# Optimization experiments

Measured on AMD Instinct MI355X. Metric: run time of the kernel, lower is better.

The kernel has to match this reference:

```python
import jax, jax.numpy as jnp
import numpy as np


def _mlp(x, W1, b1, W2, b2):
    # x: (B, M, T); torch MLPLayer: transpose(1,2) -> Linear -> Linear -> LeakyReLU -> transpose back
    h = jnp.einsum('bmt,hm->bht', x, W1) + b1[None, :, None]   # (B, H, T)
    y = jnp.einsum('bht,oh->bot', h, W2) + b2[None, :, None]   # (B, M, T)
    return jax.nn.leaky_relu(y, negative_slope=0.01)


def _calc_attn(q, k, v):
    # q: (B, M, Tq), k: (B, M, Tk), v: (B, M, Tk)
    Tq = q.shape[-1]
    qk = jnp.einsum('bmq,bmk->bqk', q, k)                       # (B, Tq, Tk)
    eye = jnp.eye(Tq, dtype=qk.dtype)                           # broadcasts: (Tq,Tq) or (1,1)
    logits = jnp.exp(qk - qk * eye / jnp.sqrt(jnp.asarray(Tq, qk.dtype)))
    scores = jax.nn.softmax(logits, axis=-1)
    return jnp.einsum('bqk,bmk->bmq', scores, v)                # (B, M, Tq)


def setup_inputs() -> dict:
    key = jax.random.key(0)
    B, M, T, H = 16, 128, 2048, 512
    ks = jax.random.split(key, 14)
    s = 0.02
    inp = {
        'pattern': jax.random.normal(ks[0], (B, M, T), jnp.float32),
        'value': jax.random.normal(ks[1], (B, M, T), jnp.float32),
        'kernel_size': 33,
    }
    names = ['q', 'k', 'o']
    for i, n in enumerate(names):
        inp['W%s1' % n] = jax.random.normal(ks[2 + 4 * i], (H, M), jnp.float32) * s
        inp['b%s1' % n] = jax.random.normal(ks[3 + 4 * i], (H,), jnp.float32) * s
        inp['W%s2' % n] = jax.random.normal(ks[4 + 4 * i], (M, H), jnp.float32) * s
        inp['b%s2' % n] = jax.random.normal(ks[5 + 4 * i], (M,), jnp.float32) * s
    return inp


def reference(pattern, value, kernel_size, Wq1, bq1, Wq2, bq2, Wk1, bk1, Wk2, bk2, Wo1, bo1, Wo2, bo2):
    query = _mlp(pattern, Wq1, bq1, Wq2, bq2)
    key = _mlp(pattern, Wk1, bk1, Wk2, bk2)
    # full (internal) attention
    attn_in = _calc_attn(query, key, value)                     # (B, M, T)
    rep_in = _mlp(attn_in, Wo1, bo1, Wo2, bo2)
    # windowed (external) attention
    T = query.shape[-1]
    cu = (kernel_size - 1) // 2
    q_w = query[..., T - 1 - cu : T - cu]                       # (B, M, 1)
    k_w = key[..., kernel_size - cu - 1 : T - cu - 2]           # (B, M, T-k-1)
    v_w = value[..., kernel_size : T - 1]                       # (B, M, T-k-1)
    attn_ex = _calc_attn(q_w, k_w, v_w)                         # (B, M, 1)
    rep_ex = _mlp(attn_ex, Wo1, bo1, Wo2, bo2)
    return jnp.concatenate([rep_in, rep_ex], axis=-1)           # (B, M, T+1)
```

## Files before the change

### kernel.cpp

```cpp
#include <hip/hip_runtime.h>
#include <math.h>

#define B_    16
#define M_    128
#define T_    2048
#define H_    512
#define TOUT_ 2049

typedef unsigned short u16;
typedef unsigned int   u32;
typedef __bf16 bf16x8 __attribute__((ext_vector_type(8)));
typedef float  f32x16 __attribute__((ext_vector_type(16)));
typedef u32    u32x4  __attribute__((ext_vector_type(4)));
typedef u32    u32x2  __attribute__((ext_vector_type(2)));

#define A_OFF     0
#define C_OFF     16384
#define MEAN_OFF  16896
#define AQKBF_OFF 19200
#define AOBF_OFF  35584
#define QT_OFF    43776
#define KT_OFF    (43776 + 2097152)
#define VB_OFF    (43776 + 2 * 2097152)

static __device__ __forceinline__ u16 f2bf(float f) {
  u32 u = __float_as_uint(f);
  u = (u + 0x7FFFu + ((u >> 16) & 1u)) >> 16;
  return (u16)u;
}
static __device__ __forceinline__ u32 pk2(float lo, float hi) {
  return (u32)f2bf(lo) | ((u32)f2bf(hi) << 16);
}
static __device__ __forceinline__ bf16x8 ldfrag(const u16* p) {
  return __builtin_bit_cast(bf16x8, *(const u32x4*)p);
}

__global__ __launch_bounds__(128) void fuse_weights_all(
    const float* __restrict__ W1q, const float* __restrict__ b1q,
    const float* __restrict__ W2q, const float* __restrict__ b2q,
    const float* __restrict__ W1k, const float* __restrict__ b1k,
    const float* __restrict__ W2k, const float* __restrict__ b2k,
    const float* __restrict__ W1o, const float* __restrict__ b1o,
    const float* __restrict__ W2o, const float* __restrict__ b2o,
    float* __restrict__ A, float* __restrict__ c,
    u16* __restrict__ Aqk_bf, u16* __restrict__ Ao_bf) {
  __shared__ float w2row[H_];
  int which = blockIdx.x >> 7;
  int o = blockIdx.x & 127;
  const float* W1 = which == 0 ? W1q : which == 1 ? W1k : W1o;
  const float* b1 = which == 0 ? b1q : which == 1 ? b1k : b1o;
  const float* W2 = which == 0 ? W2q : which == 1 ? W2k : W2o;
  const float* b2 = which == 0 ? b2q : which == 1 ? b2k : b2o;
  int m = threadIdx.x;
  for (int h = m; h < H_; h += 128) w2row[h] = W2[o * H_ + h];
  __syncthreads();
  float acc = 0.f;
#pragma unroll 8
  for (int h = 0; h < H_; ++h) acc = fmaf(w2row[h], W1[h * M_ + m], acc);
  u16 ab = f2bf(acc);
  if (which == 0)      Aqk_bf[o * 128 + m] = ab;
  else if (which == 1) Aqk_bf[(128 + o) * 128 + m] = ab;
  else               { Ao_bf[o * 128 + m] = ab; A[o * M_ + m] = acc; }
  if (m < 64) {
    float cc = 0.f;
    for (int h = m; h < H_; h += 64) cc = fmaf(w2row[h], b1[h], cc);
#pragma unroll
    for (int off = 32; off > 0; off >>= 1) cc += __shfl_down(cc, off, 64);
    if (m == 0) c[which * 128 + o] = cc + b2[o];
  }
}

#define XS 68

__global__ __launch_bounds__(256) void prep_kernel(
    const float* __restrict__ pattern, const u16* __restrict__ Aqk_bf,
    const float* __restrict__ cqk, u16* __restrict__ qT, u16* __restrict__ kT,
    const float* __restrict__ value, u16* __restrict__ vb,
    float* __restrict__ meanv) {
  __shared__ alignas(16) float xsf[128 * XS];
  int bx = blockIdx.x;
  int tid = threadIdx.x;

  if (bx >= 512) {
    int bm = bx - 512;
    float* red = xsf;
    const float* row = value + (size_t)bm * T_;
    int i0 = tid * 8;
    float4 a = *(const float4*)(row + i0);
    float4 bq = *(const float4*)(row + i0 + 4);
    u32x4 o = {pk2(a.x, a.y), pk2(a.z, a.w), pk2(bq.x, bq.y), pk2(bq.z, bq.w)};
    *(u32x4*)&vb[(size_t)bm * T_ + i0] = o;
    float vals[8] = {a.x, a.y, a.z, a.w, bq.x, bq.y, bq.z, bq.w};
    float s = 0.f;
#pragma unroll
    for (int j = 0; j < 8; ++j) {
      int idx = i0 + j;
      if (idx >= 33 && idx < T_ - 1) s += vals[j];
    }
    red[tid] = s;
    __syncthreads();
    for (int st = 128; st > 0; st >>= 1) {
      if (tid < st) red[tid] += red[tid + st];
      __syncthreads();
    }
    if (tid == 0) meanv[bm] = red[0] * (1.f / 2014.f);
    return;
  }

  int b = bx >> 5;
  int t0 = (bx & 31) * 64;
  int lane = tid & 63;
  int wv = tid >> 6;
  int l31 = lane & 31;
  int lh8 = (lane >> 5) * 8;

  bf16x8 afr[2][8];
#pragma unroll
  for (int i = 0; i < 2; ++i) {
    const u16* ap = Aqk_bf + ((2 * wv + i) * 32 + l31) * 128 + lh8;
#pragma unroll
    for (int s = 0; s < 8; ++s) afr[i][s] = ldfrag(ap + 16 * s);
  }

#pragma unroll
  for (int rep = 0; rep < 8; ++rep) {
    int m = rep * 16 + (tid >> 4);
    int tc = (tid & 15) * 4;
    float4 v = *(const float4*)&pattern[(size_t)(b * M_ + m) * T_ + t0 + tc];
    *(float4*)&xsf[m * XS + tc] = v;
  }
  __syncthreads();

  bf16x8 bfr[2][8];
#pragma unroll
  for (int tt = 0; tt < 2; ++tt) {
#pragma unroll
    for (int s = 0; s < 8; ++s) {
      float v0 = xsf[(s * 16 + lh8 + 0) * XS + tt * 32 + l31];
      float v1 = xsf[(s * 16 + lh8 + 1) * XS + tt * 32 + l31];
      float v2 = xsf[(s * 16 + lh8 + 2) * XS + tt * 32 + l31];
      float v3 = xsf[(s * 16 + lh8 + 3) * XS + tt * 32 + l31];
      float v4 = xsf[(s * 16 + lh8 + 4) * XS + tt * 32 + l31];
      float v5 = xsf[(s * 16 + lh8 + 5) * XS + tt * 32 + l31];
      float v6 = xsf[(s * 16 + lh8 + 6) * XS + tt * 32 + l31];
      float v7 = xsf[(s * 16 + lh8 + 7) * XS + tt * 32 + l31];
      u32x4 p = {pk2(v0, v1), pk2(v2, v3), pk2(v4, v5), pk2(v6, v7)};
      bfr[tt][s] = __builtin_bit_cast(bf16x8, p);
    }
  }
  __syncthreads();

  u16* obuf = (u16*)xsf;
#pragma unroll
  for (int tt = 0; tt < 2; ++tt) {
#pragma unroll
    for (int i = 0; i < 2; ++i) {
      f32x16 acc;
#pragma unroll
      for (int r = 0; r < 16; ++r) acc[r] = 0.f;
#pragma unroll
      for (int s = 0; s < 8; ++s)
        acc = __builtin_amdgcn_mfma_f32_32x32x16_bf16(afr[i][s], bfr[tt][s], acc, 0, 0, 0);
      int ot = 2 * wv + i;
      int t = tt * 32 + l31;
#pragma unroll
      for (int r = 0; r < 16; ++r) {
        int orow = (r & 3) + 8 * (r >> 2) + 4 * (lane >> 5);
        float v = acc[r] + cqk[ot * 32 + orow];
        v = v > 0.f ? v : 0.01f * v;
        obuf[t * 258 + ot * 32 + orow] = f2bf(v);
      }
    }
  }
  __syncthreads();

  const u32* ob32 = (const u32*)obuf;
#pragma unroll
  for (int g = 0; g < 8; ++g) {
    int G = wv * 8 + g;
    int mat = G >> 4;
    int t = (G & 15) * 4 + (lane >> 4);
    int og2 = lane & 15;
    int wbase = t * 129 + mat * 64 + og2 * 4;
    u32x4 vv = {ob32[wbase], ob32[wbase + 1], ob32[wbase + 2], ob32[wbase + 3]};
    u32* dst = (u32*)((mat ? kT : qT) + ((size_t)(b * T_ + t0 + t)) * 128) + og2 * 4;
    *(u32x4*)dst = vv;
  }
}

#define QSTR 136
#define VSTR 72

__global__ __launch_bounds__(256, 2) void attn_mfma_kernel(
    const u16* __restrict__ qT, const u16* __restrict__ kT,
    const u16* __restrict__ vB, const u16* __restrict__ Ao_bf,
    const float* __restrict__ co, const float* __restrict__ Aofp,
    const float* __restrict__ meanv, float* __restrict__ out) {
  __shared__ alignas(16) u16 qsw[64 * QSTR];
  __shared__ alignas(16) u16 ks[64 * QSTR];
  __shared__ alignas(16) u16 vs[2][128 * VSTR];
  __shared__ float dls[128];

  int b = blockIdx.y;
  int q0 = blockIdx.x * 64;
  int tid = threadIdx.x;
  int lane = tid & 63;
  int wv = tid >> 6;
  int l31 = lane & 31;
  int lh8 = (lane >> 5) * 8;

  {
    const u16* gq = qT + (size_t)(b * T_ + q0) * 128;
#pragma unroll
    for (int it = 0; it < 4; ++it) {
      int r = it * 16 + (tid >> 4);
      int cm = (tid & 15) * 8;
      *(u32x4*)&qsw[r * QSTR + cm] = *(const u32x4*)&gq[r * 128 + cm];
    }
  }

  const u16* gkb = kT + (size_t)b * T_ * 128;
  const u16* gvb = vB + (size_t)b * M_ * T_;
  int kr = tid >> 4, kc = (tid & 15) * 8;
  int vr = tid >> 3, vc = (tid & 7) * 8;

  u32x4 kreg[4], vreg[4];
#pragma unroll
  for (int it = 0; it < 4; ++it) {
    kreg[it] = *(const u32x4*)&gkb[(size_t)(it * 16 + kr) * 128 + kc];
    vreg[it] = *(const u32x4*)&gvb[(size_t)(it * 32 + vr) * T_ + vc];
  }

  __syncthreads();

  int qw = (wv >> 1) * 32;
  int kw = (wv & 1) * 32;
  bf16x8 afrag[8];
  {
    const u16* qrow = &qsw[(qw + l31) * QSTR + lh8];
#pragma unroll
    for (int s = 0; s < 8; ++s) afrag[s] = ldfrag(qrow + s * 16);
  }

  int qt = wv & 1;
  int mb = (wv >> 1) * 2;

#pragma unroll
  for (int it = 0; it < 4; ++it) {
    *(u32x4*)&ks[(it * 16 + kr) * QSTR + kc] = kreg[it];
    *(u32x4*)&vs[0][(it * 32 + vr) * VSTR + vc] = vreg[it];
  }
#pragma unroll
  for (int it = 0; it < 4; ++it) {
    kreg[it] = *(const u32x4*)&gkb[(size_t)(64 + it * 16 + kr) * 128 + kc];
    vreg[it] = *(const u32x4*)&gvb[(size_t)(it * 32 + vr) * T_ + 64 + vc];
  }

  f32x16 pacc[2];
  float dreg[16];
#pragma unroll
  for (int i = 0; i < 16; ++i) { pacc[0][i] = 0.f; pacc[1][i] = 0.f; dreg[i] = 0.f; }

  for (int kt = 0; kt < T_ / 64; ++kt) {
    int k0 = kt * 64;
    int cur = kt & 1;
    __syncthreads();

    f32x16 sacc;
#pragma unroll
    for (int i = 0; i < 16; ++i) sacc[i] = 0.f;
    {
      const u16* krow = &ks[(kw + l31) * QSTR + lh8];
#pragma unroll
      for (int s = 0; s < 8; ++s) {
        bf16x8 bf = ldfrag(krow + s * 16);
        sacc = __builtin_amdgcn_mfma_f32_32x32x16_bf16(afrag[s], bf, sacc, 0, 0, 0);
      }
    }

    int kl = kw + l31;
    if (k0 == q0) {
#pragma unroll
      for (int r = 0; r < 16; ++r) {
        int qrow = qw + (r & 3) + 8 * (r >> 2) + 4 * (lane >> 5);
        if (qrow == kl) sacc[r] *= 0.97790291f;
      }
    }
#pragma unroll
    for (int r = 0; r < 16; ++r) {
      int qrow = qw + (r & 3) + 8 * (r >> 2) + 4 * (lane >> 5);
      float w = __expf(__expf(sacc[r]));
      u16 wb = f2bf(w);
      dreg[r] += __uint_as_float((u32)wb << 16);
      qsw[qrow * VSTR + kl] = wb;
    }
    __syncthreads();

    if (kt < T_ / 64 - 1) {
#pragma unroll
      for (int it = 0; it < 4; ++it) {
        *(u32x4*)&ks[(it * 16 + kr) * QSTR + kc] = kreg[it];
        *(u32x4*)&vs[1 - cur][(it * 32 + vr) * VSTR + vc] = vreg[it];
      }
      int kn = (kt + 2 < T_ / 64) ? (kt + 2) * 64 : k0 + 64;
#pragma unroll
      for (int it = 0; it < 4; ++it) {
        kreg[it] = *(const u32x4*)&gkb[(size_t)(kn + it * 16 + kr) * 128 + kc];
        vreg[it] = *(const u32x4*)&gvb[(size_t)(it * 32 + vr) * T_ + kn + vc];
      }
    }

#pragma unroll
    for (int s2 = 0; s2 < 4; ++s2) {
      bf16x8 wf = ldfrag(&qsw[(qt * 32 + l31) * VSTR + s2 * 16 + lh8]);
      bf16x8 vf0 = ldfrag(&vs[cur][(mb * 32 + l31) * VSTR + s2 * 16 + lh8]);
      bf16x8 vf1 = ldfrag(&vs[cur][((mb + 1) * 32 + l31) * VSTR + s2 * 16 + lh8]);
      pacc[0] = __builtin_amdgcn_mfma_f32_32x32x16_bf16(vf0, wf, pacc[0], 0, 0, 0);
      pacc[1] = __builtin_amdgcn_mfma_f32_32x32x16_bf16(vf1, wf, pacc[1], 0, 0, 0);
    }
  }

#pragma unroll
  for (int r = 0; r < 16; ++r) {
    float d = dreg[r];
    for (int off = 1; off < 32; off <<= 1) d += __shfl_xor(d, off, 64);
    dreg[r] = d;
  }
  if (l31 == 0) {
#pragma unroll
    for (int r = 0; r < 16; ++r) {
      int qrow = qw + (r & 3) + 8 * (r >> 2) + 4 * (lane >> 5);
      dls[(wv & 1) * 64 + qrow] = dreg[r];
    }
  }
  __syncthreads();

  {
    int qcol = qt * 32 + l31;
    float rden = 1.f / (dls[qcol] + dls[64 + qcol]);
#pragma unroll
    for (int mi = 0; mi < 2; ++mi) {
      int mbase = (mb + mi) * 32 + 4 * (lane >> 5);
#pragma unroll
      for (int g = 0; g < 4; ++g) {
        float v0 = pacc[mi][4 * g + 0] * rden;
        float v1 = pacc[mi][4 * g + 1] * rden;
        float v2 = pacc[mi][4 * g + 2] * rden;
        float v3 = pacc[mi][4 * g + 3] * rden;
        u32x2 w = {pk2(v0, v1), pk2(v2, v3)};
        *(u32x2*)&qsw[qcol * QSTR + mbase + 8 * g] = w;
      }
    }
  }
  __syncthreads();

  bf16x8 aofr[8];
  {
    const u16* ap = Ao_bf + (wv * 32 + l31) * 128 + lh8;
#pragma unroll
    for (int s = 0; s < 8; ++s) aofr[s] = ldfrag(ap + 16 * s);
  }
#pragma unroll
  for (int qt2 = 0; qt2 < 2; ++qt2) {
    bf16x8 pfr[8];
    const u16* pp = &qsw[(qt2 * 32 + l31) * QSTR + lh8];
#pragma unroll
    for (int s = 0; s < 8; ++s) pfr[s] = ldfrag(pp + 16 * s);
    f32x16 oacc;
#pragma unroll
    for (int r = 0; r < 16; ++r) oacc[r] = 0.f;
#pragma unroll
    for (int s = 0; s < 8; ++s)
      oacc = __builtin_amdgcn_mfma_f32_32x32x16_bf16(aofr[s], pfr[s], oacc, 0, 0, 0);
#pragma unroll
    for (int r = 0; r < 16; ++r) {
      int orow = wv * 32 + (r & 3) + 8 * (r >> 2) + 4 * (lane >> 5);
      float v = oacc[r] + co[orow];
      v = v > 0.f ? v : 0.01f * v;
      out[((size_t)(b * M_ + orow)) * TOUT_ + q0 + qt2 * 32 + l31] = v;
    }
  }

  if (q0 == 0 && tid < 128) {
    float acc = co[tid];
    const float* mv = meanv + b * 128;
    for (int m = 0; m < 128; ++m) acc = fmaf(Aofp[tid * 128 + m], mv[m], acc);
    acc = acc > 0.f ? acc : 0.01f * acc;
    out[((size_t)(b * M_ + tid)) * TOUT_ + 2048] = acc;
  }
}

extern "C" void kernel_launch(void* const* d_in, const int* in_sizes, int n_in,
                              void* d_out, int out_size, void* d_ws, size_t ws_size,
                              hipStream_t stream) {
  (void)in_sizes; (void)n_in; (void)out_size; (void)ws_size;
  const float* pattern = (const float*)d_in[0];
  const float* value   = (const float*)d_in[1];
  const float* Wq1 = (const float*)d_in[3];
  const float* bq1 = (const float*)d_in[4];
  const float* Wq2 = (const float*)d_in[5];
  const float* bq2 = (const float*)d_in[6];
  const float* Wk1 = (const float*)d_in[7];
  const float* bk1 = (const float*)d_in[8];
  const float* Wk2 = (const float*)d_in[9];
  const float* bk2 = (const float*)d_in[10];
  const float* Wo1 = (const float*)d_in[11];
  const float* bo1 = (const float*)d_in[12];
  const float* Wo2 = (const float*)d_in[13];
  const float* bo2 = (const float*)d_in[14];

  float* ws     = (float*)d_ws;
  float* A      = ws + A_OFF;
  float* c      = ws + C_OFF;
  float* meanv  = ws + MEAN_OFF;
  u16*   Aqk_bf = (u16*)(ws + AQKBF_OFF);
  u16*   Ao_bf  = (u16*)(ws + AOBF_OFF);
  u16*   qT     = (u16*)(ws + QT_OFF);
  u16*   kT     = (u16*)(ws + KT_OFF);
  u16*   vB     = (u16*)(ws + VB_OFF);
  float* out    = (float*)d_out;

  fuse_weights_all<<<384, 128, 0, stream>>>(
      Wq1, bq1, Wq2, bq2, Wk1, bk1, Wk2, bk2, Wo1, bo1, Wo2, bo2,
      A, c, Aqk_bf, Ao_bf);

  prep_kernel<<<512 + B_ * M_, 256, 0, stream>>>(
      pattern, Aqk_bf, c, qT, kT, value, vB, meanv);

  attn_mfma_kernel<<<dim3(T_ / 64, B_), 256, 0, stream>>>(
      qT, kT, vB, Ao_bf, c + 256, A, meanv, out);
}
```

Baseline: 202.0 us.

## Widen attention query tile to 128 with 8-wave blocks sharing K/V tiles

```diff
diff --git a/kernel.cpp b/kernel.cpp
--- a/kernel.cpp
+++ b/kernel.cpp
@@ -1,4 +1,5 @@
 #include <hip/hip_runtime.h>
+#include <hip/hip_bf16.h>
 #include <math.h>
 
 #define B_    16
@@ -29,7 +30,10 @@
   return (u16)u;
 }
 static __device__ __forceinline__ u32 pk2(float lo, float hi) {
-  return (u32)f2bf(lo) | ((u32)f2bf(hi) << 16);
+  __hip_bfloat162 h = __float22bfloat162_rn(float2{lo, hi});
+  u32 r;
+  __builtin_memcpy(&r, &h, 4);
+  return r;
 }
 static __device__ __forceinline__ bf16x8 ldfrag(const u16* p) {
   return __builtin_bit_cast(bf16x8, *(const u32x4*)p);
@@ -190,19 +194,22 @@
 
 #define QSTR 136
 #define VSTR 72
-
-__global__ __launch_bounds__(256, 2) void attn_mfma_kernel(
+#define NKT  (T_ / 64)
+
+__global__ __launch_bounds__(512, 2) void attn_mfma_kernel(
     const u16* __restrict__ qT, const u16* __restrict__ kT,
     const u16* __restrict__ vB, const u16* __restrict__ Ao_bf,
     const float* __restrict__ co, const float* __restrict__ Aofp,
     const float* __restrict__ meanv, float* __restrict__ out) {
-  __shared__ alignas(16) u16 qsw[64 * QSTR];
-  __shared__ alignas(16) u16 ks[64 * QSTR];
-  __shared__ alignas(16) u16 vs[2][128 * VSTR];
-  __shared__ float dls[128];
+  extern __shared__ u16 smem[];
+  u16* qsw = smem;
+  u16* ks  = smem + 128 * QSTR;
+  u16* vs0 = ks + 64 * QSTR;
+  u16* vs1 = vs0 + 128 * VSTR;
+  float* dls = (float*)(vs1 + 128 * VSTR);
 
   int b = blockIdx.y;
-  int q0 = blockIdx.x * 64;
+  int q0 = blockIdx.x * 128;
   int tid = threadIdx.x;
   int lane = tid & 63;
   int wv = tid >> 6;
@@ -213,7 +220,7 @@
     const u16* gq = qT + (size_t)(b * T_ + q0) * 128;
 #pragma unroll
     for (int it = 0; it < 4; ++it) {
-      int r = it * 16 + (tid >> 4);
+      int r = it * 32 + (tid >> 4);
       int cm = (tid & 15) * 8;
       *(u32x4*)&qsw[r * QSTR + cm] = *(const u32x4*)&gq[r * 128 + cm];
     }
@@ -224,17 +231,17 @@
   int kr = tid >> 4, kc = (tid & 15) * 8;
   int vr = tid >> 3, vc = (tid & 7) * 8;
 
-  u32x4 kreg[4], vreg[4];
-#pragma unroll
-  for (int it = 0; it < 4; ++it) {
-    kreg[it] = *(const u32x4*)&gkb[(size_t)(it * 16 + kr) * 128 + kc];
-    vreg[it] = *(const u32x4*)&gvb[(size_t)(it * 32 + vr) * T_ + vc];
-  }
-
-  __syncthreads();
-
-  int qw = (wv >> 1) * 32;
-  int kw = (wv & 1) * 32;
+  u32x4 kreg[2], vreg[2];
+#pragma unroll
+  for (int it = 0; it < 2; ++it) {
+    kreg[it] = *(const u32x4*)&gkb[(size_t)(it * 32 + kr) * 128 + kc];
+    vreg[it] = *(const u32x4*)&gvb[(size_t)(it * 64 + vr) * T_ + vc];
+  }
+
+  __syncthreads();
+
+  int qw = (wv & 3) * 32;
+  int kw = (wv >> 2) * 32;
   bf16x8 afrag[8];
   {
     const u16* qrow = &qsw[(qw + l31) * QSTR + lh8];
@@ -242,18 +249,18 @@
     for (int s = 0; s < 8; ++s) afrag[s] = ldfrag(qrow + s * 16);
   }
 
-  int qt = wv & 1;
-  int mb = (wv >> 1) * 2;
-
-#pragma unroll
-  for (int it = 0; it < 4; ++it) {
-    *(u32x4*)&ks[(it * 16 + kr) * QSTR + kc] = kreg[it];
-    *(u32x4*)&vs[0][(it * 32 + vr) * VSTR + vc] = vreg[it];
-  }
-#pragma unroll
-  for (int it = 0; it < 4; ++it) {
-    kreg[it] = *(const u32x4*)&gkb[(size_t)(64 + it * 16 + kr) * 128 + kc];
-    vreg[it] = *(const u32x4*)&gvb[(size_t)(it * 32 + vr) * T_ + 64 + vc];
+  int qt = wv & 3;
+  int mb = (wv >> 2) * 2;
+
+#pragma unroll
+  for (int it = 0; it < 2; ++it) {
+    *(u32x4*)&ks[(it * 32 + kr) * QSTR + kc] = kreg[it];
+    *(u32x4*)&vs0[(it * 64 + vr) * VSTR + vc] = vreg[it];
+  }
+#pragma unroll
+  for (int it = 0; it < 2; ++it) {
+    kreg[it] = *(const u32x4*)&gkb[(size_t)(64 + it * 32 + kr) * 128 + kc];
+    vreg[it] = *(const u32x4*)&gvb[(size_t)(it * 64 + vr) * T_ + 64 + vc];
   }
 
   f32x16 pacc[2];
@@ -261,9 +268,10 @@
 #pragma unroll
   for (int i = 0; i < 16; ++i) { pacc[0][i] = 0.f; pacc[1][i] = 0.f; dreg[i] = 0.f; }
 
-  for (int kt = 0; kt < T_ / 64; ++kt) {
+  for (int kt = 0; kt < NKT; ++kt) {
     int k0 = kt * 64;
-    int cur = kt & 1;
+    u16* vcur = (kt & 1) ? vs1 : vs0;
+    u16* vnxt = (kt & 1) ? vs0 : vs1;
     __syncthreads();
 
     f32x16 sacc;
@@ -279,42 +287,45 @@
     }
 
     int kl = kw + l31;
-    if (k0 == q0) {
+    if (q0 + qw == k0 + kw) {
 #pragma unroll
       for (int r = 0; r < 16; ++r) {
         int qrow = qw + (r & 3) + 8 * (r >> 2) + 4 * (lane >> 5);
-        if (qrow == kl) sacc[r] *= 0.97790291f;
-      }
-    }
-#pragma unroll
-    for (int r = 0; r < 16; ++r) {
+        if (qrow == kl + (k0 - q0)) sacc[r] *= 0.97790291f;
+      }
+    }
+#pragma unroll
+    for (int r = 0; r < 16; r += 2) {
       int qrow = qw + (r & 3) + 8 * (r >> 2) + 4 * (lane >> 5);
-      float w = __expf(__expf(sacc[r]));
-      u16 wb = f2bf(w);
-      dreg[r] += __uint_as_float((u32)wb << 16);
-      qsw[qrow * VSTR + kl] = wb;
+      float w0 = __expf(__expf(sacc[r]));
+      float w1 = __expf(__expf(sacc[r + 1]));
+      u32 p = pk2(w0, w1);
+      dreg[r]     += __uint_as_float(p << 16);
+      dreg[r + 1] += __uint_as_float(p & 0xffff0000u);
+      qsw[qrow * VSTR + kl]       = (u16)p;
+      qsw[(qrow + 1) * VSTR + kl] = (u16)(p >> 16);
     }
     __syncthreads();
 
-    if (kt < T_ / 64 - 1) {
-#pragma unroll
-      for (int it = 0; it < 4; ++it) {
-        *(u32x4*)&ks[(it * 16 + kr) * QSTR + kc] = kreg[it];
-        *(u32x4*)&vs[1 - cur][(it * 32 + vr) * VSTR + vc] = vreg[it];
-      }
-      int kn = (kt + 2 < T_ / 64) ? (kt + 2) * 64 : k0 + 64;
-#pragma unroll
-      for (int it = 0; it < 4; ++it) {
-        kreg[it] = *(const u32x4*)&gkb[(size_t)(kn + it * 16 + kr) * 128 + kc];
-        vreg[it] = *(const u32x4*)&gvb[(size_t)(it * 32 + vr) * T_ + kn + vc];
+    if (kt < NKT - 1) {
+#pragma unroll
+      for (int it = 0; it < 2; ++it) {
+        *(u32x4*)&ks[(it * 32 + kr) * QSTR + kc] = kreg[it];
+        *(u32x4*)&vnxt[(it * 64 + vr) * VSTR + vc] = vreg[it];
+      }
+      int kn = (kt + 2 < NKT) ? (kt + 2) * 64 : (NKT - 1) * 64;
+#pragma unroll
+      for (int it = 0; it < 2; ++it) {
+        kreg[it] = *(const u32x4*)&gkb[(size_t)(kn + it * 32 + kr) * 128 + kc];
+        vreg[it] = *(const u32x4*)&gvb[(size_t)(it * 64 + vr) * T_ + kn + vc];
       }
     }
 
 #pragma unroll
     for (int s2 = 0; s2 < 4; ++s2) {
       bf16x8 wf = ldfrag(&qsw[(qt * 32 + l31) * VSTR + s2 * 16 + lh8]);
-      bf16x8 vf0 = ldfrag(&vs[cur][(mb * 32 + l31) * VSTR + s2 * 16 + lh8]);
-      bf16x8 vf1 = ldfrag(&vs[cur][((mb + 1) * 32 + l31) * VSTR + s2 * 16 + lh8]);
+      bf16x8 vf0 = ldfrag(&vcur[(mb * 32 + l31) * VSTR + s2 * 16 + lh8]);
+      bf16x8 vf1 = ldfrag(&vcur[((mb + 1) * 32 + l31) * VSTR + s2 * 16 + lh8]);
       pacc[0] = __builtin_amdgcn_mfma_f32_32x32x16_bf16(vf0, wf, pacc[0], 0, 0, 0);
       pacc[1] = __builtin_amdgcn_mfma_f32_32x32x16_bf16(vf1, wf, pacc[1], 0, 0, 0);
     }
@@ -330,14 +341,14 @@
 #pragma unroll
     for (int r = 0; r < 16; ++r) {
       int qrow = qw + (r & 3) + 8 * (r >> 2) + 4 * (lane >> 5);
-      dls[(wv & 1) * 64 + qrow] = dreg[r];
+      dls[(wv >> 2) * 128 + qrow] = dreg[r];
     }
   }
   __syncthreads();
 
   {
     int qcol = qt * 32 + l31;
-    float rden = 1.f / (dls[qcol] + dls[64 + qcol]);
+    float rden = 1.f / (dls[qcol] + dls[128 + qcol]);
 #pragma unroll
     for (int mi = 0; mi < 2; ++mi) {
       int mbase = (mb + mi) * 32 + 4 * (lane >> 5);
@@ -356,12 +367,13 @@
 
   bf16x8 aofr[8];
   {
-    const u16* ap = Ao_bf + (wv * 32 + l31) * 128 + lh8;
+    const u16* ap = Ao_bf + ((wv & 3) * 32 + l31) * 128 + lh8;
 #pragma unroll
     for (int s = 0; s < 8; ++s) aofr[s] = ldfrag(ap + 16 * s);
   }
 #pragma unroll
-  for (int qt2 = 0; qt2 < 2; ++qt2) {
+  for (int j = 0; j < 2; ++j) {
+    int qt2 = (wv >> 2) * 2 + j;
     bf16x8 pfr[8];
     const u16* pp = &qsw[(qt2 * 32 + l31) * QSTR + lh8];
 #pragma unroll
@@ -374,14 +386,14 @@
       oacc = __builtin_amdgcn_mfma_f32_32x32x16_bf16(aofr[s], pfr[s], oacc, 0, 0, 0);
 #pragma unroll
     for (int r = 0; r < 16; ++r) {
-      int orow = wv * 32 + (r & 3) + 8 * (r >> 2) + 4 * (lane >> 5);
+      int orow = (wv & 3) * 32 + (r & 3) + 8 * (r >> 2) + 4 * (lane >> 5);
       float v = oacc[r] + co[orow];
       v = v > 0.f ? v : 0.01f * v;
       out[((size_t)(b * M_ + orow)) * TOUT_ + q0 + qt2 * 32 + l31] = v;
     }
   }
 
-  if (q0 == 0 && tid < 128) {
+  if (blockIdx.x == 0 && tid < 128) {
     float acc = co[tid];
     const float* mv = meanv + b * 128;
     for (int m = 0; m < 128; ++m) acc = fmaf(Aofp[tid * 128 + m], mv[m], acc);
@@ -427,6 +439,8 @@
   prep_kernel<<<512 + B_ * M_, 256, 0, stream>>>(
       pattern, Aqk_bf, c, qT, kT, value, vB, meanv);
 
-  attn_mfma_kernel<<<dim3(T_ / 64, B_), 256, 0, stream>>>(
+  size_t lds_bytes = (128 * QSTR + 64 * QSTR + 2 * 128 * VSTR) * sizeof(u16)
+                   + 256 * sizeof(float);
+  attn_mfma_kernel<<<dim3(T_ / 128, B_), 512, lds_bytes, stream>>>(
       qT, kT, vB, Ao_bf, c + 256, A, meanv, out);
 }
```

After: 192.8 us. 1.05x faster.
